# Kernel optimization log

Measured on AMD Instinct MI355X. Metric: run time of the kernel, lower is better.

## Reference

```python
import jax, jax.numpy as jnp
import numpy as np

N, E, NG = 50000, 800000, 256          # nodes, edges, graphs
NODE, EDGE, HID, OUT = 64, 16, 64, 1   # feature dims
NUM_LAYERS = 3


def _lin(key, fan_in, fan_out):
    # torch Linear default init: U(-1/sqrt(fan_in), 1/sqrt(fan_in))
    kw, kb = jax.random.split(key)
    bound = 1.0 / np.sqrt(fan_in)
    W = jax.random.uniform(kw, (fan_in, fan_out), jnp.float32, -bound, bound)
    b = jax.random.uniform(kb, (fan_out,), jnp.float32, -bound, bound)
    return W, b


def setup_inputs() -> dict:
    key = jax.random.key(0)
    ks = jax.random.split(key, 8)
    x = jax.random.normal(ks[0], (N, NODE), jnp.float32)
    edge_attr = jax.random.normal(ks[1], (E, EDGE), jnp.float32)
    edge_index = jax.random.randint(ks[2], (2, E), 0, N, dtype=jnp.int32)
    batch = jnp.sort(jax.random.randint(ks[3], (N,), 0, NG, dtype=jnp.int32))
    W_nh, b_nh = _lin(ks[4], NODE, HID)                 # node_to_hidden
    W_mh, b_mh = _lin(ks[5], 2 * HID + EDGE, HID)       # message_to_hidden
    W_om, b_om = _lin(ks[6], 2 * HID + NODE, HID)       # outMsgLin
    W_out, b_out = _lin(ks[7], HID, OUT)                # outLin
    return {"x": x, "edge_attr": edge_attr,
            "W_nh": W_nh, "b_nh": b_nh, "W_mh": W_mh, "b_mh": b_mh,
            "W_om": W_om, "b_om": b_om, "W_out": W_out, "b_out": b_out,
            "edge_index": edge_index, "batch": batch}


def reference(x, edge_attr, W_nh, b_nh, W_mh, b_mh, W_om, b_om, W_out, b_out,
              edge_index, batch):
    # h0 = relu(node_to_hidden(x))
    h0 = jax.nn.relu(x @ W_nh + b_nh)                      # [N, HID]

    # add_self_loops: append N self edges, self-loop edge_attr filled with 1.0
    self_idx = jnp.arange(N, dtype=edge_index.dtype)
    src = jnp.concatenate([edge_index[0], self_idx])       # x_j index (source)
    dst = jnp.concatenate([edge_index[1], self_idx])       # x_i index (target)
    ea = jnp.concatenate([edge_attr,
                          jnp.ones((N, EDGE), edge_attr.dtype)], axis=0)

    # MPN: num_layers of gather-concat -> scatter-add -> linear + h0 -> relu
    h = h0
    for _ in range(NUM_LAYERS):
        msg = jnp.concatenate([h[dst], h[src], ea], axis=1)        # [E+N, 2H+EDGE]
        agg = jax.ops.segment_sum(msg, dst, num_segments=N)        # [N, 2H+EDGE]
        h = jax.nn.relu(agg @ W_mh + b_mh + h0)                    # [N, HID]

    # outMsg: message = concat[h_i, h_j, x_j], aggr add, update identity
    out_msg = jnp.concatenate([h[dst], h[src], x[src]], axis=1)    # [E+N, 2H+NODE]
    agg2 = jax.ops.segment_sum(out_msg, dst, num_segments=N)       # [N, 2H+NODE]

    out = jax.nn.relu(agg2 @ W_om + b_om)                          # [N, HID]
    pooled = jax.ops.segment_sum(out, batch, num_segments=NG)      # [NG, HID]
    return pooled @ W_out + b_out                                  # [NG, OUT]
```

## Files before the change

### kernel.cpp

```cpp
#include <hip/hip_runtime.h>
#include <hip/hip_fp16.h>

#define N_NODES 50000
#define N_EDGES 800000
#define NGRAPH  256
#define FDIM    64
#define EDIM    16
#define NT      (N_NODES / 16)
#define SH      8
#define M8      (N_NODES * SH)
#define NB8     ((M8 + 255) / 256)
#define CH8     ((NB8 + 255) / 256)

#define GRPS       8
#define GRP_BLOCKS 256
#define GRID_CF    (GRPS * GRP_BLOCKS)
#define NPG        ((N_NODES + GRPS - 1) / GRPS)

#define SRC_SHARD(s) ((s) >> 13)

using half8  = __attribute__((ext_vector_type(8))) _Float16;
using float4v = __attribute__((ext_vector_type(4))) float;

__device__ __forceinline__ unsigned hadd2u(unsigned a, unsigned b) {
    __half2 r = __hadd2(__builtin_bit_cast(__half2, a), __builtin_bit_cast(__half2, b));
    return __builtin_bit_cast(unsigned, r);
}
__device__ __forceinline__ unsigned hmul2u(unsigned a, __half2 m) {
    __half2 r = __hmul2(__builtin_bit_cast(__half2, a), m);
    return __builtin_bit_cast(unsigned, r);
}
__device__ __forceinline__ unsigned packf2(float a, float b) {
    return __builtin_bit_cast(unsigned, __floats2half2_rn(a, b));
}


__global__ __launch_bounds__(256) void k_count(const int* __restrict__ src,
                                               const int* __restrict__ dst,
                                               int* __restrict__ cnt8) {
    int grp = blockIdx.x & (GRPS - 1);
    int bi  = blockIdx.x >> 3;
    int lo = grp * NPG;
    int hi = lo + NPG; if (hi > N_NODES) hi = N_NODES;
    for (int e = bi * 256 + threadIdx.x; e < N_EDGES; e += GRP_BLOCKS * 256) {
        int d = dst[e];
        if (d >= lo && d < hi) atomicAdd(&cnt8[d * SH + SRC_SHARD(src[e])], 1);
    }
}

__global__ void k_cvt_x(const float* __restrict__ x, __half* __restrict__ x16) {
    int t = blockIdx.x * blockDim.x + threadIdx.x;
    if (t < N_NODES * FDIM) x16[t] = __float2half(x[t]);
}

__global__ void k_blksum(const int* __restrict__ cnt8, int* __restrict__ blksum) {
    __shared__ int red[4];
    int b = blockIdx.x, t = threadIdx.x;
    int idx = b * 256 + t;
    int s = (idx < M8) ? cnt8[idx] : 0;
#pragma unroll
    for (int off = 32; off > 0; off >>= 1) s += __shfl_down(s, off, 64);
    int lane = t & 63, wid = t >> 6;
    if (lane == 0) red[wid] = s;
    __syncthreads();
    if (t == 0) blksum[b] = red[0] + red[1] + red[2] + red[3];
}

__global__ void k_scanblk(const int* __restrict__ blksum, int* __restrict__ boff,
                          int* __restrict__ rowp8) {
    __shared__ int sh[256];
    int t = threadIdx.x;
    int base = t * CH8;
    int v[CH8];
    int s = 0;
#pragma unroll
    for (int i = 0; i < CH8; i++) {
        int idx = base + i;
        v[i] = (idx < NB8) ? blksum[idx] : 0;
        s += v[i];
    }
    sh[t] = s;
    __syncthreads();
    for (int off = 1; off < 256; off <<= 1) {
        int u = (t >= off) ? sh[t - off] : 0;
        __syncthreads();
        sh[t] += u;
        __syncthreads();
    }
    int run = (t == 0) ? 0 : sh[t - 1];
#pragma unroll
    for (int i = 0; i < CH8; i++) {
        int idx = base + i;
        if (idx < NB8) boff[idx] = run;
        run += v[i];
    }
    if (t == 255) rowp8[M8] = sh[255];
}

__global__ void k_rowp(const int* __restrict__ cnt8, const int* __restrict__ boff,
                       int* __restrict__ rowp8, int* __restrict__ cur8) {
    __shared__ int sh[256];
    int b = blockIdx.x, t = threadIdx.x;
    int idx = b * 256 + t;
    int v = (idx < M8) ? cnt8[idx] : 0;
    sh[t] = v;
    __syncthreads();
    for (int off = 1; off < 256; off <<= 1) {
        int u = (t >= off) ? sh[t - off] : 0;
        __syncthreads();
        sh[t] += u;
        __syncthreads();
    }
    if (idx < M8) {
        int excl = sh[t] - v + boff[b];
        rowp8[idx] = excl;
        cur8[idx]  = excl;
    }
}

__global__ void k_degf(const int* __restrict__ rowp8, float* __restrict__ degf) {
    int i = blockIdx.x * blockDim.x + threadIdx.x;
    if (i < N_NODES) degf[i] = (float)(rowp8[(i + 1) * SH] - rowp8[i * SH] + 1);
}

__global__ __launch_bounds__(256) void k_fill(const int* __restrict__ src,
                                              const int* __restrict__ dst,
                                              int* __restrict__ cur8,
                                              int* __restrict__ colsrc,
                                              int* __restrict__ coledge) {
    int grp = blockIdx.x & (GRPS - 1);
    int bi  = blockIdx.x >> 3;
    int lo = grp * NPG;
    int hi = lo + NPG; if (hi > N_NODES) hi = N_NODES;
    for (int e = bi * 256 + threadIdx.x; e < N_EDGES; e += GRP_BLOCKS * 256) {
        int d = dst[e];
        if (d >= lo && d < hi) {
            int s = src[e];
            int pos = atomicAdd(&cur8[d * SH + SRC_SHARD(s)], 1);
            colsrc[pos]  = s;
            coledge[pos] = e;
        }
    }
}

#define SROW 136

__global__ __launch_bounds__(256, 4) void k_gmv(
    const __half* __restrict__ hin16,
    const int* __restrict__ rowp8, const int* __restrict__ colsrc,
    const __half* __restrict__ base16, const float* __restrict__ degf,
    const float* __restrict__ Wmh, __half* __restrict__ hout16) {
    __shared__ __align__(16) _Float16 S[4][16 * SROW];
    int lane = threadIdx.x & 63, wid = threadIdx.x >> 6;
    int t = blockIdx.x * 4 + wid;
    if (t >= NT) return;
    int tb = t * 16;
    int g = lane >> 3;
    int c = lane & 7;
    const uint4* h8 = (const uint4*)hin16;

#pragma unroll
    for (int pass = 0; pass < 2; pass++) {
        int m = pass * 8 + g;
        int node = tb + m;
        int beg = rowp8[node * SH], end = rowp8[(node + 1) * SH];
        float a0 = 0, a1 = 0, a2 = 0, a3 = 0, a4 = 0, a5 = 0, a6 = 0, a7 = 0;
        for (int p = beg; p < end; p += 8) {
            int cidx = p + c; if (cidx > end - 1) cidx = end - 1;
            int vj = colsrc[cidx];
#pragma unroll
            for (int k = 0; k < 8; k++) {
                int j = __shfl(vj, g * 8 + k, 64);
                if (p + k < end) {
                    uint4 v = h8[(size_t)j * 8 + c];
                    float2 f0 = __half22float2(__builtin_bit_cast(__half2, v.x));
                    float2 f1 = __half22float2(__builtin_bit_cast(__half2, v.y));
                    float2 f2 = __half22float2(__builtin_bit_cast(__half2, v.z));
                    float2 f3 = __half22float2(__builtin_bit_cast(__half2, v.w));
                    a0 += f0.x; a1 += f0.y; a2 += f1.x; a3 += f1.y;
                    a4 += f2.x; a5 += f2.y; a6 += f3.x; a7 += f3.y;
                }
            }
        }
        uint4 hv = h8[(size_t)node * 8 + c];
        float dg = degf[node];
        __half dh = __float2half(dg);
        __half2 dh2 = __halves2half2(dh, dh);
        float2 f0 = __half22float2(__builtin_bit_cast(__half2, hv.x));
        float2 f1 = __half22float2(__builtin_bit_cast(__half2, hv.y));
        float2 f2 = __half22float2(__builtin_bit_cast(__half2, hv.z));
        float2 f3 = __half22float2(__builtin_bit_cast(__half2, hv.w));
        uint4 s2, s1;
        s2.x = packf2(a0 + f0.x, a1 + f0.y);
        s2.y = packf2(a2 + f1.x, a3 + f1.y);
        s2.z = packf2(a4 + f2.x, a5 + f2.y);
        s2.w = packf2(a6 + f3.x, a7 + f3.y);
        s1.x = hmul2u(hv.x, dh2); s1.y = hmul2u(hv.y, dh2);
        s1.z = hmul2u(hv.z, dh2); s1.w = hmul2u(hv.w, dh2);
        uint4* Sw = (uint4*)(&S[wid][m * SROW]);
        Sw[c]     = s2;
        Sw[8 + c] = s1;
    }

    int n = lane & 15, quad = lane >> 4;
    half8 bfr[4][4];
#pragma unroll
    for (int kk = 0; kk < 4; kk++)
#pragma unroll
        for (int nn = 0; nn < 4; nn++) {
            half8 tmp;
#pragma unroll
            for (int j = 0; j < 8; j++) {
                int kp = kk * 32 + quad * 8 + j;
                int krow = (kp < 64) ? (64 + kp) : (kp - 64);
                tmp[j] = (_Float16)Wmh[krow * FDIM + nn * 16 + n];
            }
            bfr[kk][nn] = tmp;
        }
    float4v acc[4];
#pragma unroll
    for (int nn = 0; nn < 4; nn++)
#pragma unroll
        for (int r = 0; r < 4; r++)
            acc[nn][r] = __half2float(base16[(size_t)(tb + quad * 4 + r) * FDIM + nn * 16 + n]);
    const _Float16* Sr = S[wid];
#pragma unroll
    for (int kk = 0; kk < 4; kk++) {
        half8 a = *(const half8*)(Sr + n * SROW + kk * 32 + quad * 8);
#pragma unroll
        for (int nn = 0; nn < 4; nn++)
            acc[nn] = __builtin_amdgcn_mfma_f32_16x16x32_f16(a, bfr[kk][nn], acc[nn], 0, 0, 0);
    }
#pragma unroll
    for (int nn = 0; nn < 4; nn++)
#pragma unroll
        for (int r = 0; r < 4; r++)
            hout16[(size_t)(tb + quad * 4 + r) * FDIM + nn * 16 + n] =
                __float2half(fmaxf(acc[nn][r], 0.f));
}

__global__ __launch_bounds__(256, 4) void k_gout(
    const __half* __restrict__ hin16,
    const int* __restrict__ rowp8, const int* __restrict__ colsrc,
    const __half* __restrict__ obase16, const float* __restrict__ degf,
    const float* __restrict__ Wom, const float* __restrict__ Wout,
    float* __restrict__ sc) {
    __shared__ __align__(16) _Float16 S[4][16 * SROW];
    int lane = threadIdx.x & 63, wid = threadIdx.x >> 6;
    int t = blockIdx.x * 4 + wid;
    if (t >= NT) return;
    int tb = t * 16;
    int g = lane >> 3;
    int c = lane & 7;
    const uint4* h8 = (const uint4*)hin16;

#pragma unroll
    for (int pass = 0; pass < 2; pass++) {
        int m = pass * 8 + g;
        int node = tb + m;
        int beg = rowp8[node * SH], end = rowp8[(node + 1) * SH];
        float a0 = 0, a1 = 0, a2 = 0, a3 = 0, a4 = 0, a5 = 0, a6 = 0, a7 = 0;
        for (int p = beg; p < end; p += 8) {
            int cidx = p + c; if (cidx > end - 1) cidx = end - 1;
            int vj = colsrc[cidx];
#pragma unroll
            for (int k = 0; k < 8; k++) {
                int j = __shfl(vj, g * 8 + k, 64);
                if (p + k < end) {
                    uint4 v = h8[(size_t)j * 8 + c];
                    float2 f0 = __half22float2(__builtin_bit_cast(__half2, v.x));
                    float2 f1 = __half22float2(__builtin_bit_cast(__half2, v.y));
                    float2 f2 = __half22float2(__builtin_bit_cast(__half2, v.z));
                    float2 f3 = __half22float2(__builtin_bit_cast(__half2, v.w));
                    a0 += f0.x; a1 += f0.y; a2 += f1.x; a3 += f1.y;
                    a4 += f2.x; a5 += f2.y; a6 += f3.x; a7 += f3.y;
                }
            }
        }
        uint4 hv = h8[(size_t)node * 8 + c];
        float dg = degf[node];
        __half dh = __float2half(dg);
        __half2 dh2 = __halves2half2(dh, dh);
        float2 f0 = __half22float2(__builtin_bit_cast(__half2, hv.x));
        float2 f1 = __half22float2(__builtin_bit_cast(__half2, hv.y));
        float2 f2 = __half22float2(__builtin_bit_cast(__half2, hv.z));
        float2 f3 = __half22float2(__builtin_bit_cast(__half2, hv.w));
        uint4 s2, s1;
        s2.x = packf2(a0 + f0.x, a1 + f0.y);
        s2.y = packf2(a2 + f1.x, a3 + f1.y);
        s2.z = packf2(a4 + f2.x, a5 + f2.y);
        s2.w = packf2(a6 + f3.x, a7 + f3.y);
        s1.x = hmul2u(hv.x, dh2); s1.y = hmul2u(hv.y, dh2);
        s1.z = hmul2u(hv.z, dh2); s1.w = hmul2u(hv.w, dh2);
        uint4* Sw = (uint4*)(&S[wid][m * SROW]);
        Sw[c]     = s2;
        Sw[8 + c] = s1;
    }

    int n = lane & 15, quad = lane >> 4;
    half8 bfr[4][4];
#pragma unroll
    for (int kk = 0; kk < 4; kk++)
#pragma unroll
        for (int nn = 0; nn < 4; nn++) {
            half8 tmp;
#pragma unroll
            for (int j = 0; j < 8; j++) {
                int kp = kk * 32 + quad * 8 + j;
                int krow = (kp < 64) ? (64 + kp) : (kp - 64);
                tmp[j] = (_Float16)Wom[krow * FDIM + nn * 16 + n];
            }
            bfr[kk][nn] = tmp;
        }
    float wo0 = Wout[n], wo1 = Wout[16 + n], wo2 = Wout[32 + n], wo3 = Wout[48 + n];
    float4v acc[4];
#pragma unroll
    for (int nn = 0; nn < 4; nn++)
#pragma unroll
        for (int r = 0; r < 4; r++)
            acc[nn][r] = __half2float(obase16[(size_t)(tb + quad * 4 + r) * FDIM + nn * 16 + n]);
    const _Float16* Sr = S[wid];
#pragma unroll
    for (int kk = 0; kk < 4; kk++) {
        half8 a = *(const half8*)(Sr + n * SROW + kk * 32 + quad * 8);
#pragma unroll
        for (int nn = 0; nn < 4; nn++)
            acc[nn] = __builtin_amdgcn_mfma_f32_16x16x32_f16(a, bfr[kk][nn], acc[nn], 0, 0, 0);
    }
#pragma unroll
    for (int r = 0; r < 4; r++) {
        float s = fmaxf(acc[0][r], 0.f) * wo0 + fmaxf(acc[1][r], 0.f) * wo1
                + fmaxf(acc[2][r], 0.f) * wo2 + fmaxf(acc[3][r], 0.f) * wo3;
        s += __shfl_xor(s, 1, 64);
        s += __shfl_xor(s, 2, 64);
        s += __shfl_xor(s, 4, 64);
        s += __shfl_xor(s, 8, 64);
        if (n == 0) sc[tb + quad * 4 + r] = s;
    }
}

#define SROW2 72
__global__ __launch_bounds__(256, 4) void k_gxob(
    const __half* __restrict__ x16, const float* __restrict__ edge_attr,
    const int* __restrict__ rowp8, const int* __restrict__ colsrc,
    const int* __restrict__ coledge,
    const float* __restrict__ Wom, const float* __restrict__ bom,
    __half* __restrict__ obase16, float* __restrict__ ea) {
    __shared__ __align__(16) _Float16 S[4][16 * SROW2];
    int lane = threadIdx.x & 63, wid = threadIdx.x >> 6;
    int t = blockIdx.x * 4 + wid;
    if (t >= NT) return;
    int tb = t * 16;
    int g = lane >> 3;
    int c = lane & 7;
    const uint4* h8 = (const uint4*)x16;
    const float2* a2p = (const float2*)edge_attr;

#pragma unroll
    for (int pass = 0; pass < 2; pass++) {
        int m = pass * 8 + g;
        int node = tb + m;
        int beg = rowp8[node * SH], end = rowp8[(node + 1) * SH];
        float a0 = 0, a1 = 0, a2 = 0, a3 = 0, a4 = 0, a5 = 0, a6 = 0, a7 = 0;
        float x0 = 0.f, x1 = 0.f;
        for (int p = beg; p < end; p += 8) {
            int cidx = p + c; if (cidx > end - 1) cidx = end - 1;
            int vs = colsrc[cidx];
            int ve = coledge[cidx];
#pragma unroll
            for (int k = 0; k < 8; k++) {
                int j = __shfl(vs, g * 8 + k, 64);
                int e = __shfl(ve, g * 8 + k, 64);
                if (p + k < end) {
                    uint4 v = h8[(size_t)j * 8 + c];
                    float2 w = a2p[(size_t)e * 8 + c];
                    float2 f0 = __half22float2(__builtin_bit_cast(__half2, v.x));
                    float2 f1 = __half22float2(__builtin_bit_cast(__half2, v.y));
                    float2 f2 = __half22float2(__builtin_bit_cast(__half2, v.z));
                    float2 f3 = __half22float2(__builtin_bit_cast(__half2, v.w));
                    a0 += f0.x; a1 += f0.y; a2 += f1.x; a3 += f1.y;
                    a4 += f2.x; a5 += f2.y; a6 += f3.x; a7 += f3.y;
                    x0 += w.x; x1 += w.y;
                }
            }
        }
        uint4 xv = h8[(size_t)node * 8 + c];
        float2 f0 = __half22float2(__builtin_bit_cast(__half2, xv.x));
        float2 f1 = __half22float2(__builtin_bit_cast(__half2, xv.y));
        float2 f2 = __half22float2(__builtin_bit_cast(__half2, xv.z));
        float2 f3 = __half22float2(__builtin_bit_cast(__half2, xv.w));
        uint4 sA;
        sA.x = packf2(a0 + f0.x, a1 + f0.y);
        sA.y = packf2(a2 + f1.x, a3 + f1.y);
        sA.z = packf2(a4 + f2.x, a5 + f2.y);
        sA.w = packf2(a6 + f3.x, a7 + f3.y);
        uint4* Sw = (uint4*)(&S[wid][m * SROW2]);
        Sw[c] = sA;
        ((float2*)ea)[(size_t)node * 8 + c] = make_float2(x0, x1);
    }

    int n = lane & 15, quad = lane >> 4;
    half8 bfr[2][4];
#pragma unroll
    for (int kk = 0; kk < 2; kk++)
#pragma unroll
        for (int nn = 0; nn < 4; nn++) {
            half8 tmp;
#pragma unroll
            for (int j = 0; j < 8; j++) {
                int kp = kk * 32 + quad * 8 + j;
                tmp[j] = (_Float16)Wom[(128 + kp) * FDIM + nn * 16 + n];
            }
            bfr[kk][nn] = tmp;
        }
    float bom_n[4];
#pragma unroll
    for (int nn = 0; nn < 4; nn++) bom_n[nn] = bom[nn * 16 + n];
    float4v acc[4];
#pragma unroll
    for (int nn = 0; nn < 4; nn++)
#pragma unroll
        for (int r = 0; r < 4; r++) acc[nn][r] = bom_n[nn];
    const _Float16* Sr = S[wid];
#pragma unroll
    for (int kk = 0; kk < 2; kk++) {
        half8 a = *(const half8*)(Sr + n * SROW2 + kk * 32 + quad * 8);
#pragma unroll
        for (int nn = 0; nn < 4; nn++)
            acc[nn] = __builtin_amdgcn_mfma_f32_16x16x32_f16(a, bfr[kk][nn], acc[nn], 0, 0, 0);
    }
#pragma unroll
    for (int nn = 0; nn < 4; nn++)
#pragma unroll
        for (int r = 0; r < 4; r++)
            obase16[(size_t)(tb + quad * 4 + r) * FDIM + nn * 16 + n] =
                __float2half(acc[nn][r]);
}

__global__ void k_h0base(const float* __restrict__ x, const float* __restrict__ ea,
                         const float* __restrict__ Wnh, const float* __restrict__ bnh,
                         const float* __restrict__ Wmh, const float* __restrict__ bmh,
                         __half* __restrict__ h0out16, __half* __restrict__ base16) {
    __shared__ __align__(16) float sx[4][FDIM];
    __shared__ __align__(16) float sea[4][EDIM];
    int lane = threadIdx.x & 63;
    int wid  = threadIdx.x >> 6;
    float wnh[FDIM], w3[EDIM];
#pragma unroll
    for (int m = 0; m < FDIM; m++) wnh[m] = Wnh[m * FDIM + lane];
    float csum = 0.f;
#pragma unroll
    for (int m = 0; m < EDIM; m++) {
        w3[m] = Wmh[(2 * FDIM + m) * FDIM + lane];
        csum += w3[m];
    }
    float bnhk = bnh[lane], bmhk = bmh[lane];
    int gw = blockIdx.x * 4 + wid;
    int nw = gridDim.x * 4;
    for (int i = gw; i < N_NODES; i += nw) {
        sx[wid][lane] = x[i * FDIM + lane];
        if (lane < EDIM) sea[wid][lane] = ea[i * EDIM + lane];
        float acc0 = bnhk, acc1 = 0.f, acc2 = 0.f, acc3 = 0.f;
        const float4* s4 = (const float4*)sx[wid];
#pragma unroll
        for (int m4 = 0; m4 < FDIM / 4; m4++) {
            float4 v = s4[m4];
            acc0 = fmaf(v.x, wnh[4 * m4 + 0], acc0);
            acc1 = fmaf(v.y, wnh[4 * m4 + 1], acc1);
            acc2 = fmaf(v.z, wnh[4 * m4 + 2], acc2);
            acc3 = fmaf(v.w, wnh[4 * m4 + 3], acc3);
        }
        float h0 = fmaxf((acc0 + acc2) + (acc1 + acc3), 0.f);
        float b0 = h0 + bmhk + csum, b1 = 0.f, b2 = 0.f, b3 = 0.f;
        const float4* e4 = (const float4*)sea[wid];
#pragma unroll
        for (int m4 = 0; m4 < EDIM / 4; m4++) {
            float4 v = e4[m4];
            b0 = fmaf(v.x, w3[4 * m4 + 0], b0);
            b1 = fmaf(v.y, w3[4 * m4 + 1], b1);
            b2 = fmaf(v.z, w3[4 * m4 + 2], b2);
            b3 = fmaf(v.w, w3[4 * m4 + 3], b3);
        }
        h0out16[i * FDIM + lane] = __float2half(h0);
        base16[i * FDIM + lane]  = __float2half((b0 + b2) + (b1 + b3));
    }
}

__global__ void k_pool(const float* __restrict__ sc, const int* __restrict__ batch,
                       const float* __restrict__ b_out, float* __restrict__ out) {
    __shared__ float red[4];
    int g = blockIdx.x, t = threadIdx.x;
    int lo = 0, hi = N_NODES;
    while (lo < hi) { int mid = (lo + hi) >> 1; if (batch[mid] < g) lo = mid + 1; else hi = mid; }
    int lo2 = lo, hi2 = N_NODES;
    while (lo2 < hi2) { int mid = (lo2 + hi2) >> 1; if (batch[mid] < g + 1) lo2 = mid + 1; else hi2 = mid; }
    float s = 0.f;
    for (int i = lo + t; i < lo2; i += 256) s += sc[i];
#pragma unroll
    for (int off = 32; off > 0; off >>= 1) s += __shfl_down(s, off, 64);
    int lane = t & 63, wid = t >> 6;
    if (lane == 0) red[wid] = s;
    __syncthreads();
    if (t == 0) out[g] = red[0] + red[1] + red[2] + red[3] + b_out[0];
}


extern "C" void kernel_launch(void* const* d_in, const int* in_sizes, int n_in,
                              void* d_out, int out_size, void* d_ws, size_t ws_size,
                              hipStream_t stream) {
    const float* x         = (const float*)d_in[0];
    const float* edge_attr = (const float*)d_in[1];
    const float* Wnh       = (const float*)d_in[2];
    const float* bnh       = (const float*)d_in[3];
    const float* Wmh       = (const float*)d_in[4];
    const float* bmh       = (const float*)d_in[5];
    const float* Wom       = (const float*)d_in[6];
    const float* bom       = (const float*)d_in[7];
    const float* Wout      = (const float*)d_in[8];
    const float* bout      = (const float*)d_in[9];
    const int*   eidx      = (const int*)d_in[10];
    const int*   batch     = (const int*)d_in[11];
    const int*   srcI = eidx;
    const int*   dstI = eidx + N_EDGES;
    float* out = (float*)d_out;
    (void)in_sizes; (void)n_in; (void)out_size;

    char* w = (char*)d_ws;
    size_t off = 0;
    auto take = [&](size_t b) -> void* {
        void* p = w + off;
        off = (off + b + 255) & ~(size_t)255;
        return p;
    };
    float*  ea     = (float*)take((size_t)N_NODES * EDIM * 4);
    int*    cnt8   = (int*)take((size_t)M8 * 4);
    int*    rowp8  = (int*)take((size_t)(M8 + 1) * 4);
    int*    cur8   = (int*)take((size_t)M8 * 4);
    float*  degf   = (float*)take((size_t)N_NODES * 4);
    int*    colsrc = (int*)take((size_t)N_EDGES * 4);
    int*    coledge= (int*)take((size_t)N_EDGES * 4);
    float*  sc     = (float*)take((size_t)N_NODES * 4);
    int*    blks   = (int*)take((size_t)NB8 * 4);
    int*    boff   = (int*)take((size_t)NB8 * 4);
    __half* x16    = (__half*)take((size_t)N_NODES * FDIM * 2);
    __half* hA16   = (__half*)take((size_t)N_NODES * FDIM * 2);
    __half* hB16   = (__half*)take((size_t)N_NODES * FDIM * 2);
    __half* base16 = (__half*)take((size_t)N_NODES * FDIM * 2);
    __half* obase16= (__half*)take((size_t)N_NODES * FDIM * 2);
    (void)ws_size;

    const int MVG = (NT + 3) / 4;

    hipMemsetAsync(cnt8, 0, (size_t)M8 * 4, stream);
    k_count<<<GRID_CF, 256, 0, stream>>>(srcI, dstI, cnt8);
    k_cvt_x<<<(N_NODES * FDIM + 255) / 256, 256, 0, stream>>>(x, x16);
    k_blksum<<<NB8, 256, 0, stream>>>(cnt8, blks);
    k_scanblk<<<1, 256, 0, stream>>>(blks, boff, rowp8);
    k_rowp<<<NB8, 256, 0, stream>>>(cnt8, boff, rowp8, cur8);
    k_degf<<<(N_NODES + 255) / 256, 256, 0, stream>>>(rowp8, degf);
    k_fill<<<GRID_CF, 256, 0, stream>>>(srcI, dstI, cur8, colsrc, coledge);

    k_gxob<<<MVG, 256, 0, stream>>>(x16, edge_attr, rowp8, colsrc, coledge,
                                    Wom, bom, obase16, ea);
    k_h0base<<<2048, 256, 0, stream>>>(x, ea, Wnh, bnh, Wmh, bmh, hA16, base16);

    k_gmv<<<MVG, 256, 0, stream>>>(hA16, rowp8, colsrc, base16, degf, Wmh, hB16);
    k_gmv<<<MVG, 256, 0, stream>>>(hB16, rowp8, colsrc, base16, degf, Wmh, hA16);
    k_gmv<<<MVG, 256, 0, stream>>>(hA16, rowp8, colsrc, base16, degf, Wmh, hB16);

    k_gout<<<MVG, 256, 0, stream>>>(hB16, rowp8, colsrc, obase16, degf, Wom, Wout, sc);
    k_pool<<<NGRAPH, 256, 0, stream>>>(sc, batch, bout, out);
}
```

Measured before the change: 371.3 us.

## Split each node tile across two waves and pre-permute fp16 edge attributes in CSR order

Gather/MFMA kernels now assign two waves per 16-node tile: each wave gathers 8 nodes, they exchange through shared memory with a block barrier, and each computes half the output columns. This doubles the wave count so more gathers are in flight. Separately, the CSR fill step writes edge attributes as fp16 in CSR order, so the out-message kernel streams them contiguously instead of doing an indirect fp32 gather through edge ids. The cost is an extra barrier per block, a split bias trick in k_gout, and a larger scattered write in the fill step.

Result: faster. 361.2 us (-2.7%).

```diff
diff --git a/kernel.cpp b/kernel.cpp
--- a/kernel.cpp
+++ b/kernel.cpp
@@ -22,10 +22,6 @@
 using half8  = __attribute__((ext_vector_type(8))) _Float16;
 using float4v = __attribute__((ext_vector_type(4))) float;
 
-__device__ __forceinline__ unsigned hadd2u(unsigned a, unsigned b) {
-    __half2 r = __hadd2(__builtin_bit_cast(__half2, a), __builtin_bit_cast(__half2, b));
-    return __builtin_bit_cast(unsigned, r);
-}
 __device__ __forceinline__ unsigned hmul2u(unsigned a, __half2 m) {
     __half2 r = __hmul2(__builtin_bit_cast(__half2, a), m);
     return __builtin_bit_cast(unsigned, r);
@@ -125,9 +121,10 @@
 
 __global__ __launch_bounds__(256) void k_fill(const int* __restrict__ src,
                                               const int* __restrict__ dst,
+                                              const float* __restrict__ edge_attr,
                                               int* __restrict__ cur8,
                                               int* __restrict__ colsrc,
-                                              int* __restrict__ coledge) {
+                                              __half* __restrict__ colea) {
     int grp = blockIdx.x & (GRPS - 1);
     int bi  = blockIdx.x >> 3;
     int lo = grp * NPG;
@@ -137,8 +134,16 @@
         if (d >= lo && d < hi) {
             int s = src[e];
             int pos = atomicAdd(&cur8[d * SH + SRC_SHARD(s)], 1);
-            colsrc[pos]  = s;
-            coledge[pos] = e;
+            colsrc[pos] = s;
+            const float4* ap = (const float4*)(edge_attr + (size_t)e * EDIM);
+            float4 w0 = ap[0], w1 = ap[1], w2 = ap[2], w3 = ap[3];
+            uint4 h0, h1;
+            h0.x = packf2(w0.x, w0.y); h0.y = packf2(w0.z, w0.w);
+            h0.z = packf2(w1.x, w1.y); h0.w = packf2(w1.z, w1.w);
+            h1.x = packf2(w2.x, w2.y); h1.y = packf2(w2.z, w2.w);
+            h1.z = packf2(w3.x, w3.y); h1.w = packf2(w3.z, w3.w);
+            uint4* cp = (uint4*)(colea + (size_t)pos * EDIM);
+            cp[0] = h0; cp[1] = h1;
         }
     }
 }
@@ -150,18 +155,17 @@
     const int* __restrict__ rowp8, const int* __restrict__ colsrc,
     const __half* __restrict__ base16, const float* __restrict__ degf,
     const float* __restrict__ Wmh, __half* __restrict__ hout16) {
-    __shared__ __align__(16) _Float16 S[4][16 * SROW];
+    __shared__ __align__(16) _Float16 S[2][16 * SROW];
     int lane = threadIdx.x & 63, wid = threadIdx.x >> 6;
-    int t = blockIdx.x * 4 + wid;
-    if (t >= NT) return;
+    int tile = wid >> 1, h = wid & 1;
+    int t = blockIdx.x * 2 + tile;
     int tb = t * 16;
     int g = lane >> 3;
     int c = lane & 7;
     const uint4* h8 = (const uint4*)hin16;
 
-#pragma unroll
-    for (int pass = 0; pass < 2; pass++) {
-        int m = pass * 8 + g;
+    if (t < NT) {
+        int m = h * 8 + g;
         int node = tb + m;
         int beg = rowp8[node * SH], end = rowp8[(node + 1) * SH];
         float a0 = 0, a1 = 0, a2 = 0, a3 = 0, a4 = 0, a5 = 0, a6 = 0, a7 = 0;
@@ -197,17 +201,20 @@
         s2.w = packf2(a6 + f3.x, a7 + f3.y);
         s1.x = hmul2u(hv.x, dh2); s1.y = hmul2u(hv.y, dh2);
         s1.z = hmul2u(hv.z, dh2); s1.w = hmul2u(hv.w, dh2);
-        uint4* Sw = (uint4*)(&S[wid][m * SROW]);
+        uint4* Sw = (uint4*)(&S[tile][m * SROW]);
         Sw[c]     = s2;
         Sw[8 + c] = s1;
     }
+    __syncthreads();
+    if (t >= NT) return;
 
     int n = lane & 15, quad = lane >> 4;
-    half8 bfr[4][4];
+    half8 bfr[4][2];
 #pragma unroll
     for (int kk = 0; kk < 4; kk++)
 #pragma unroll
-        for (int nn = 0; nn < 4; nn++) {
+        for (int i = 0; i < 2; i++) {
+            int nn = h * 2 + i;
             half8 tmp;
 #pragma unroll
             for (int j = 0; j < 8; j++) {
@@ -215,28 +222,28 @@
                 int krow = (kp < 64) ? (64 + kp) : (kp - 64);
                 tmp[j] = (_Float16)Wmh[krow * FDIM + nn * 16 + n];
             }
-            bfr[kk][nn] = tmp;
-        }
-    float4v acc[4];
-#pragma unroll
-    for (int nn = 0; nn < 4; nn++)
+            bfr[kk][i] = tmp;
+        }
+    float4v acc[2];
+#pragma unroll
+    for (int i = 0; i < 2; i++)
 #pragma unroll
         for (int r = 0; r < 4; r++)
-            acc[nn][r] = __half2float(base16[(size_t)(tb + quad * 4 + r) * FDIM + nn * 16 + n]);
-    const _Float16* Sr = S[wid];
+            acc[i][r] = __half2float(base16[(size_t)(tb + quad * 4 + r) * FDIM + (h * 2 + i) * 16 + n]);
+    const _Float16* Sr = S[tile];
 #pragma unroll
     for (int kk = 0; kk < 4; kk++) {
         half8 a = *(const half8*)(Sr + n * SROW + kk * 32 + quad * 8);
 #pragma unroll
-        for (int nn = 0; nn < 4; nn++)
-            acc[nn] = __builtin_amdgcn_mfma_f32_16x16x32_f16(a, bfr[kk][nn], acc[nn], 0, 0, 0);
-    }
-#pragma unroll
-    for (int nn = 0; nn < 4; nn++)
+        for (int i = 0; i < 2; i++)
+            acc[i] = __builtin_amdgcn_mfma_f32_16x16x32_f16(a, bfr[kk][i], acc[i], 0, 0, 0);
+    }
+#pragma unroll
+    for (int i = 0; i < 2; i++)
 #pragma unroll
         for (int r = 0; r < 4; r++)
-            hout16[(size_t)(tb + quad * 4 + r) * FDIM + nn * 16 + n] =
-                __float2half(fmaxf(acc[nn][r], 0.f));
+            hout16[(size_t)(tb + quad * 4 + r) * FDIM + (h * 2 + i) * 16 + n] =
+                __float2half(fmaxf(acc[i][r], 0.f));
 }
 
 __global__ __launch_bounds__(256, 4) void k_gout(
@@ -245,18 +252,18 @@
     const __half* __restrict__ obase16, const float* __restrict__ degf,
     const float* __restrict__ Wom, const float* __restrict__ Wout,
     float* __restrict__ sc) {
-    __shared__ __align__(16) _Float16 S[4][16 * SROW];
+    __shared__ __align__(16) _Float16 S[2][16 * SROW];
+    __shared__ float part[2][2][16];
     int lane = threadIdx.x & 63, wid = threadIdx.x >> 6;
-    int t = blockIdx.x * 4 + wid;
-    if (t >= NT) return;
+    int tile = wid >> 1, h = wid & 1;
+    int t = blockIdx.x * 2 + tile;
     int tb = t * 16;
     int g = lane >> 3;
     int c = lane & 7;
     const uint4* h8 = (const uint4*)hin16;
 
-#pragma unroll
-    for (int pass = 0; pass < 2; pass++) {
-        int m = pass * 8 + g;
+    if (t < NT) {
+        int m = h * 8 + g;
         int node = tb + m;
         int beg = rowp8[node * SH], end = rowp8[(node + 1) * SH];
         float a0 = 0, a1 = 0, a2 = 0, a3 = 0, a4 = 0, a5 = 0, a6 = 0, a7 = 0;
@@ -292,73 +299,83 @@
         s2.w = packf2(a6 + f3.x, a7 + f3.y);
         s1.x = hmul2u(hv.x, dh2); s1.y = hmul2u(hv.y, dh2);
         s1.z = hmul2u(hv.z, dh2); s1.w = hmul2u(hv.w, dh2);
-        uint4* Sw = (uint4*)(&S[wid][m * SROW]);
+        uint4* Sw = (uint4*)(&S[tile][m * SROW]);
         Sw[c]     = s2;
         Sw[8 + c] = s1;
     }
+    __syncthreads();
 
     int n = lane & 15, quad = lane >> 4;
-    half8 bfr[4][4];
-#pragma unroll
-    for (int kk = 0; kk < 4; kk++)
-#pragma unroll
-        for (int nn = 0; nn < 4; nn++) {
-            half8 tmp;
-#pragma unroll
-            for (int j = 0; j < 8; j++) {
-                int kp = kk * 32 + quad * 8 + j;
-                int krow = (kp < 64) ? (64 + kp) : (kp - 64);
-                tmp[j] = (_Float16)Wom[krow * FDIM + nn * 16 + n];
+    if (t < NT) {
+        half8 bfr[4][2];
+#pragma unroll
+        for (int kk = 0; kk < 4; kk++)
+#pragma unroll
+            for (int i = 0; i < 2; i++) {
+                int nn = h * 2 + i;
+                half8 tmp;
+#pragma unroll
+                for (int j = 0; j < 8; j++) {
+                    int kp = kk * 32 + quad * 8 + j;
+                    int krow = (kp < 64) ? (64 + kp) : (kp - 64);
+                    tmp[j] = (_Float16)Wom[krow * FDIM + nn * 16 + n];
+                }
+                bfr[kk][i] = tmp;
             }
-            bfr[kk][nn] = tmp;
-        }
-    float wo0 = Wout[n], wo1 = Wout[16 + n], wo2 = Wout[32 + n], wo3 = Wout[48 + n];
-    float4v acc[4];
-#pragma unroll
-    for (int nn = 0; nn < 4; nn++)
-#pragma unroll
-        for (int r = 0; r < 4; r++)
-            acc[nn][r] = __half2float(obase16[(size_t)(tb + quad * 4 + r) * FDIM + nn * 16 + n]);
-    const _Float16* Sr = S[wid];
-#pragma unroll
-    for (int kk = 0; kk < 4; kk++) {
-        half8 a = *(const half8*)(Sr + n * SROW + kk * 32 + quad * 8);
-#pragma unroll
-        for (int nn = 0; nn < 4; nn++)
-            acc[nn] = __builtin_amdgcn_mfma_f32_16x16x32_f16(a, bfr[kk][nn], acc[nn], 0, 0, 0);
-    }
-#pragma unroll
-    for (int r = 0; r < 4; r++) {
-        float s = fmaxf(acc[0][r], 0.f) * wo0 + fmaxf(acc[1][r], 0.f) * wo1
-                + fmaxf(acc[2][r], 0.f) * wo2 + fmaxf(acc[3][r], 0.f) * wo3;
-        s += __shfl_xor(s, 1, 64);
-        s += __shfl_xor(s, 2, 64);
-        s += __shfl_xor(s, 4, 64);
-        s += __shfl_xor(s, 8, 64);
-        if (n == 0) sc[tb + quad * 4 + r] = s;
-    }
+        float wo0 = Wout[(h * 2 + 0) * 16 + n];
+        float wo1 = Wout[(h * 2 + 1) * 16 + n];
+        float4v acc[2];
+#pragma unroll
+        for (int i = 0; i < 2; i++)
+#pragma unroll
+            for (int r = 0; r < 4; r++)
+                acc[i][r] = __half2float(obase16[(size_t)(tb + quad * 4 + r) * FDIM + (h * 2 + i) * 16 + n])
+                            * 0.5f;
+        const _Float16* Sr = S[tile];
+#pragma unroll
+        for (int kk = 0; kk < 4; kk++) {
+            half8 a = *(const half8*)(Sr + n * SROW + kk * 32 + quad * 8);
+#pragma unroll
+            for (int i = 0; i < 2; i++)
+                acc[i] = __builtin_amdgcn_mfma_f32_16x16x32_f16(a, bfr[kk][i], acc[i], 0, 0, 0);
+        }
+#pragma unroll
+        for (int r = 0; r < 4; r++) {
+            float o0 = __half2float(obase16[(size_t)(tb + quad * 4 + r) * FDIM + (h * 2 + 0) * 16 + n]);
+            float o1 = __half2float(obase16[(size_t)(tb + quad * 4 + r) * FDIM + (h * 2 + 1) * 16 + n]);
+            float v0 = acc[0][r] + o0 * 0.5f;
+            float v1 = acc[1][r] + o1 * 0.5f;
+            float s = fmaxf(v0, 0.f) * wo0 + fmaxf(v1, 0.f) * wo1;
+            s += __shfl_xor(s, 1, 64);
+            s += __shfl_xor(s, 2, 64);
+            s += __shfl_xor(s, 4, 64);
+            s += __shfl_xor(s, 8, 64);
+            if (n == 0) part[tile][h][quad * 4 + r] = s;
+        }
+    }
+    __syncthreads();
+    if (t < NT && h == 0 && lane < 16)
+        sc[tb + lane] = part[tile][0][lane] + part[tile][1][lane];
 }
 
 #define SROW2 72
 __global__ __launch_bounds__(256, 4) void k_gxob(
-    const __half* __restrict__ x16, const float* __restrict__ edge_attr,
+    const __half* __restrict__ x16, const __half* __restrict__ colea,
     const int* __restrict__ rowp8, const int* __restrict__ colsrc,
-    const int* __restrict__ coledge,
     const float* __restrict__ Wom, const float* __restrict__ bom,
     __half* __restrict__ obase16, float* __restrict__ ea) {
-    __shared__ __align__(16) _Float16 S[4][16 * SROW2];
+    __shared__ __align__(16) _Float16 S[2][16 * SROW2];
     int lane = threadIdx.x & 63, wid = threadIdx.x >> 6;
-    int t = blockIdx.x * 4 + wid;
-    if (t >= NT) return;
+    int tile = wid >> 1, h = wid & 1;
+    int t = blockIdx.x * 2 + tile;
     int tb = t * 16;
     int g = lane >> 3;
     int c = lane & 7;
     const uint4* h8 = (const uint4*)x16;
-    const float2* a2p = (const float2*)edge_attr;
-
-#pragma unroll
-    for (int pass = 0; pass < 2; pass++) {
-        int m = pass * 8 + g;
+    const unsigned* eap = (const unsigned*)colea;
+
+    if (t < NT) {
+        int m = h * 8 + g;
         int node = tb + m;
         int beg = rowp8[node * SH], end = rowp8[(node + 1) * SH];
         float a0 = 0, a1 = 0, a2 = 0, a3 = 0, a4 = 0, a5 = 0, a6 = 0, a7 = 0;
@@ -366,21 +383,20 @@
         for (int p = beg; p < end; p += 8) {
             int cidx = p + c; if (cidx > end - 1) cidx = end - 1;
             int vs = colsrc[cidx];
-            int ve = coledge[cidx];
 #pragma unroll
             for (int k = 0; k < 8; k++) {
                 int j = __shfl(vs, g * 8 + k, 64);
-                int e = __shfl(ve, g * 8 + k, 64);
                 if (p + k < end) {
                     uint4 v = h8[(size_t)j * 8 + c];
-                    float2 w = a2p[(size_t)e * 8 + c];
+                    unsigned w = eap[(size_t)(p + k) * 8 + c];
+                    float2 wf = __half22float2(__builtin_bit_cast(__half2, w));
                     float2 f0 = __half22float2(__builtin_bit_cast(__half2, v.x));
                     float2 f1 = __half22float2(__builtin_bit_cast(__half2, v.y));
                     float2 f2 = __half22float2(__builtin_bit_cast(__half2, v.z));
                     float2 f3 = __half22float2(__builtin_bit_cast(__half2, v.w));
                     a0 += f0.x; a1 += f0.y; a2 += f1.x; a3 += f1.y;
                     a4 += f2.x; a5 += f2.y; a6 += f3.x; a7 += f3.y;
-                    x0 += w.x; x1 += w.y;
+                    x0 += wf.x; x1 += wf.y;
                 }
             }
         }
@@ -394,47 +410,48 @@
         sA.y = packf2(a2 + f1.x, a3 + f1.y);
         sA.z = packf2(a4 + f2.x, a5 + f2.y);
         sA.w = packf2(a6 + f3.x, a7 + f3.y);
-        uint4* Sw = (uint4*)(&S[wid][m * SROW2]);
-        Sw[c] = sA;
+        ((uint4*)(&S[tile][m * SROW2]))[c] = sA;
         ((float2*)ea)[(size_t)node * 8 + c] = make_float2(x0, x1);
     }
+    __syncthreads();
+    if (t >= NT) return;
 
     int n = lane & 15, quad = lane >> 4;
-    half8 bfr[2][4];
+    half8 bfr[2][2];
 #pragma unroll
     for (int kk = 0; kk < 2; kk++)
 #pragma unroll
-        for (int nn = 0; nn < 4; nn++) {
+        for (int i = 0; i < 2; i++) {
+            int nn = h * 2 + i;
             half8 tmp;
 #pragma unroll
             for (int j = 0; j < 8; j++) {
                 int kp = kk * 32 + quad * 8 + j;
                 tmp[j] = (_Float16)Wom[(128 + kp) * FDIM + nn * 16 + n];
             }
-            bfr[kk][nn] = tmp;
-        }
-    float bom_n[4];
-#pragma unroll
-    for (int nn = 0; nn < 4; nn++) bom_n[nn] = bom[nn * 16 + n];
-    float4v acc[4];
-#pragma unroll
-    for (int nn = 0; nn < 4; nn++)
-#pragma unroll
-        for (int r = 0; r < 4; r++) acc[nn][r] = bom_n[nn];
-    const _Float16* Sr = S[wid];
+            bfr[kk][i] = tmp;
+        }
+    float4v acc[2];
+#pragma unroll
+    for (int i = 0; i < 2; i++) {
+        float b = bom[(h * 2 + i) * 16 + n];
+#pragma unroll
+        for (int r = 0; r < 4; r++) acc[i][r] = b;
+    }
+    const _Float16* Sr = S[tile];
 #pragma unroll
     for (int kk = 0; kk < 2; kk++) {
         half8 a = *(const half8*)(Sr + n * SROW2 + kk * 32 + quad * 8);
 #pragma unroll
-        for (int nn = 0; nn < 4; nn++)
-            acc[nn] = __builtin_amdgcn_mfma_f32_16x16x32_f16(a, bfr[kk][nn], acc[nn], 0, 0, 0);
-    }
-#pragma unroll
-    for (int nn = 0; nn < 4; nn++)
+        for (int i = 0; i < 2; i++)
+            acc[i] = __builtin_amdgcn_mfma_f32_16x16x32_f16(a, bfr[kk][i], acc[i], 0, 0, 0);
+    }
+#pragma unroll
+    for (int i = 0; i < 2; i++)
 #pragma unroll
         for (int r = 0; r < 4; r++)
-            obase16[(size_t)(tb + quad * 4 + r) * FDIM + nn * 16 + n] =
-                __float2half(acc[nn][r]);
+            obase16[(size_t)(tb + quad * 4 + r) * FDIM + (h * 2 + i) * 16 + n] =
+                __float2half(acc[i][r]);
 }
 
 __global__ void k_h0base(const float* __restrict__ x, const float* __restrict__ ea,
@@ -538,7 +555,7 @@
     int*    cur8   = (int*)take((size_t)M8 * 4);
     float*  degf   = (float*)take((size_t)N_NODES * 4);
     int*    colsrc = (int*)take((size_t)N_EDGES * 4);
-    int*    coledge= (int*)take((size_t)N_EDGES * 4);
+    __half* colea  = (__half*)take((size_t)N_EDGES * EDIM * 2);
     float*  sc     = (float*)take((size_t)N_NODES * 4);
     int*    blks   = (int*)take((size_t)NB8 * 4);
     int*    boff   = (int*)take((size_t)NB8 * 4);
@@ -549,7 +566,7 @@
     __half* obase16= (__half*)take((size_t)N_NODES * FDIM * 2);
     (void)ws_size;
 
-    const int MVG = (NT + 3) / 4;
+    const int G2 = (NT + 1) / 2;
 
     hipMemsetAsync(cnt8, 0, (size_t)M8 * 4, stream);
     k_count<<<GRID_CF, 256, 0, stream>>>(srcI, dstI, cnt8);
@@ -558,16 +575,15 @@
     k_scanblk<<<1, 256, 0, stream>>>(blks, boff, rowp8);
     k_rowp<<<NB8, 256, 0, stream>>>(cnt8, boff, rowp8, cur8);
     k_degf<<<(N_NODES + 255) / 256, 256, 0, stream>>>(rowp8, degf);
-    k_fill<<<GRID_CF, 256, 0, stream>>>(srcI, dstI, cur8, colsrc, coledge);
-
-    k_gxob<<<MVG, 256, 0, stream>>>(x16, edge_attr, rowp8, colsrc, coledge,
-                                    Wom, bom, obase16, ea);
+    k_fill<<<GRID_CF, 256, 0, stream>>>(srcI, dstI, edge_attr, cur8, colsrc, colea);
+
+    k_gxob<<<G2, 256, 0, stream>>>(x16, colea, rowp8, colsrc, Wom, bom, obase16, ea);
     k_h0base<<<2048, 256, 0, stream>>>(x, ea, Wnh, bnh, Wmh, bmh, hA16, base16);
 
-    k_gmv<<<MVG, 256, 0, stream>>>(hA16, rowp8, colsrc, base16, degf, Wmh, hB16);
-    k_gmv<<<MVG, 256, 0, stream>>>(hB16, rowp8, colsrc, base16, degf, Wmh, hA16);
-    k_gmv<<<MVG, 256, 0, stream>>>(hA16, rowp8, colsrc, base16, degf, Wmh, hB16);
-
-    k_gout<<<MVG, 256, 0, stream>>>(hB16, rowp8, colsrc, obase16, degf, Wom, Wout, sc);
+    k_gmv<<<G2, 256, 0, stream>>>(hA16, rowp8, colsrc, base16, degf, Wmh, hB16);
+    k_gmv<<<G2, 256, 0, stream>>>(hB16, rowp8, colsrc, base16, degf, Wmh, hA16);
+    k_gmv<<<G2, 256, 0, stream>>>(hA16, rowp8, colsrc, base16, degf, Wmh, hB16);
+
+    k_gout<<<G2, 256, 0, stream>>>(hB16, rowp8, colsrc, obase16, degf, Wom, Wout, sc);
     k_pool<<<NGRAPH, 256, 0, stream>>>(sc, batch, bout, out);
 }
```
